# Kernel optimization log

Hardware: AMD Instinct MI355X
Metric: run time of the kernel (lower is better)

The kernel has to match this reference:

```python
import jax, jax.numpy as jnp
import numpy as np

D_MODEL = 1024
NUM_HEADS = 16
ROPE_THETA = 10000.0


def setup_inputs() -> dict:
    key = jax.random.key(0)
    ks = jax.random.split(key, 5)
    B, S, D = 4, 2048, D_MODEL
    std = (2.0 / (D * D)) ** 0.5
    return {
        "x": jax.random.normal(ks[0], (B, S, D), dtype=jnp.float32),
        "Wq": jax.random.normal(ks[1], (D, D), dtype=jnp.float32) * std,
        "Wk": jax.random.normal(ks[2], (D, D), dtype=jnp.float32) * std,
        "Wv": jax.random.normal(ks[3], (D, D), dtype=jnp.float32) * std,
        "Wo": jax.random.normal(ks[4], (D, D), dtype=jnp.float32) * std,
    }


def _apply_rope(t, sin, cos):
    # t: [B, H, S, d_k]; sin/cos: [S, d_k//2] (broadcast over B, H)
    e = t[..., 0::2]
    o = t[..., 1::2]
    rot = jnp.stack((e * cos - o * sin, e * sin + o * cos), axis=-1)
    return rot.reshape(t.shape)  # interleave back to d_k


def reference(x, Wq, Wk, Wv, Wo):
    B, S, D = x.shape
    H = NUM_HEADS
    dk = D // H

    def proj(W):
        y = jnp.einsum('bsd,ed->bse', x, W)  # Linear: weight is [out, in]
        return y.reshape(B, S, H, dk).transpose(0, 2, 1, 3)  # [B,H,S,dk]

    q, k, v = proj(Wq), proj(Wk), proj(Wv)

    # RoPE cache (token_positions = arange(S))
    half = dk // 2
    inv_freq = 1.0 / (ROPE_THETA ** (jnp.arange(half, dtype=jnp.float32) * 2.0 / dk))
    angles = jnp.arange(S, dtype=jnp.float32)[:, None] * inv_freq[None, :]  # [S, half]
    sin, cos = jnp.sin(angles), jnp.cos(angles)
    q = _apply_rope(q, sin, cos)
    k = _apply_rope(k, sin, cos)

    # scaled dot-product attention with causal mask
    scores = jnp.einsum('bhqd,bhkd->bhqk', q, k) / jnp.sqrt(jnp.float32(dk))
    causal = jnp.tril(jnp.ones((S, S), dtype=bool))
    scores = jnp.where(causal, scores, jnp.finfo(scores.dtype).min)
    p = jax.nn.softmax(scores, axis=-1)
    out = jnp.einsum('bhqk,bhkd->bhqd', p, v)  # [B,H,S,dk]

    out = out.transpose(0, 2, 1, 3).reshape(B, S, D)
    return jnp.einsum('bsd,ed->bse', out, Wo)
```

## Files before the change

### kernel.cpp

```cpp
#include <hip/hip_runtime.h>

typedef unsigned short u16;
typedef unsigned int   u32;

typedef short    short8 __attribute__((ext_vector_type(8)));
typedef __bf16   bf16x8 __attribute__((ext_vector_type(8)));
typedef _Float16 half8  __attribute__((ext_vector_type(8)));
typedef float    f32x4  __attribute__((ext_vector_type(4)));

#define S_LEN   2048
#define DM      1024
#define NHEAD   16
#define DK      64
#define KDIM    1024

__device__ __forceinline__ u16 f2bf(float f) {
    u32 u = __builtin_bit_cast(u32, f);
    u += 0x7FFFu + ((u >> 16) & 1u);
    return (u16)(u >> 16);
}
__device__ __forceinline__ f32x4 mfma_bf16(short8 a, short8 b, f32x4 c) {
    return __builtin_amdgcn_mfma_f32_16x16x32_bf16(
        __builtin_bit_cast(bf16x8, a), __builtin_bit_cast(bf16x8, b), c, 0, 0, 0);
}
__device__ __forceinline__ f32x4 mfma_f16(half8 a, half8 b, f32x4 c) {
    return __builtin_amdgcn_mfma_f32_16x16x32_f16(a, b, c, 0, 0, 0);
}
__device__ __forceinline__ u32 pk_f16(float a, float b) {
    return __builtin_bit_cast(u32, __builtin_amdgcn_cvt_pkrtz(a, b));
}
__device__ __forceinline__ void gl_lds16(const void* g, void* l) {
    __builtin_amdgcn_global_load_lds(
        (const __attribute__((address_space(1))) u32*)g,
        (__attribute__((address_space(3))) u32*)l, 16, 0, 0);
}
__device__ __forceinline__ void bar_raw() { asm volatile("s_barrier" ::: "memory"); }
__device__ __forceinline__ void wait_vm4() { asm volatile("s_waitcnt vmcnt(4)" ::: "memory"); }
__device__ __forceinline__ void wait_vm0() { asm volatile("s_waitcnt vmcnt(0)" ::: "memory"); }

__device__ __forceinline__ int perm_inv(int rc) {
    const int nt = rc >> 4, mid = (rc >> 2) & 3, r = rc & 3;
    return 32 * (nt >> 1) + 8 * mid + 4 * (nt & 1) + r;
}

__global__ void cvt_all(const float4* __restrict__ x,  const float4* __restrict__ Wq,
                        const float4* __restrict__ Wk, const float4* __restrict__ Wv,
                        const float4* __restrict__ Wo,
                        uint2* __restrict__ oX, uint2* __restrict__ oWcat,
                        uint2* __restrict__ oWo,
                        float* __restrict__ sT, float* __restrict__ cT) {
    const int i = blockIdx.x * 256 + threadIdx.x;
    if (i < 3145728) {
        const float4* in;
        uint2* out;
        if (i < 2097152) {
            in = x + i;  out = oX + i;
        } else {
            const int j = i - 2097152;
            const int w = j >> 18, k = j & 262143;
            in  = (w == 0 ? Wq : w == 1 ? Wk : w == 2 ? Wv : Wo) + k;
            out = (w < 3) ? (oWcat + w * 262144 + k) : (oWo + k);
        }
        float4 f = *in;
        uint2 o;
        o.x = (u32)f2bf(f.x) | ((u32)f2bf(f.y) << 16);
        o.y = (u32)f2bf(f.z) | ((u32)f2bf(f.w) << 16);
        *out = o;
    } else {
        const int idx = i - 3145728;
        const float fi = expf(-(float)(idx >> 11) * 0.287823136624255f);
        const float ang = (float)(idx & 2047) * fi;
        sT[idx] = sinf(ang);
        cT[idx] = cosf(ang);
    }
}

template <int MODE>
__global__ __launch_bounds__(256)
void gemm_nt(const u16* __restrict__ A, const u16* __restrict__ Bw,
             u16* __restrict__ oQ, u16* __restrict__ oK, u16* __restrict__ oVt,
             float* __restrict__ oF,
             const float* __restrict__ ropeS, const float* __restrict__ ropeC) {
    __shared__ u16 As[2][128 * 32];
    __shared__ u16 Bs[2][128 * 32];
    const int tid  = threadIdx.x;
    const int wave = tid >> 6, lane = tid & 63;
    const int quad = lane >> 4, l15 = lane & 15;
    const int wr = wave >> 1, wc = wave & 1;
    const int NX  = (MODE == 0) ? 24 : 8;
    const int lin = (int)blockIdx.x + NX * (int)blockIdx.y;
    const int xcd = lin & 7, idx = lin >> 3;
    const int mbase = (xcd * 8 + idx / NX) * 128;
    const int nbase = (idx % NX) * 128;

    f32x4 acc[4][4];
#pragma unroll
    for (int i = 0; i < 4; i++)
#pragma unroll
        for (int j = 0; j < 4; j++) acc[i][j] = (f32x4)0.0f;

    const int srow0 = wave * 32 + (lane >> 2);
    const int srow1 = srow0 + 16;
    const int scolb = ((lane & 3) ^ ((lane >> 3) & 3)) * 16;
    const int ldsOff = wave * 2048 + lane * 16;
    const u16* gA0 = A  + (size_t)(mbase + srow0) * KDIM;
    const u16* gA1 = A  + (size_t)(mbase + srow1) * KDIM;
    const u16* gB0 = Bw + (size_t)(nbase + srow0) * KDIM;
    const u16* gB1 = Bw + (size_t)(nbase + srow1) * KDIM;
    const int koffq = (quad ^ ((l15 >> 1) & 3)) * 8;

    gl_lds16((const char*)gA0 + scolb, (char*)As[0] + ldsOff);
    gl_lds16((const char*)gA1 + scolb, (char*)As[0] + ldsOff + 1024);
    gl_lds16((const char*)gB0 + scolb, (char*)Bs[0] + ldsOff);
    gl_lds16((const char*)gB1 + scolb, (char*)Bs[0] + ldsOff + 1024);

    const int KT = KDIM / 32;
    for (int kt = 0; kt < KT; kt++) {
        const int cur = kt & 1, nxt = cur ^ 1;
        const int kkn = ((kt + 1 < KT) ? (kt + 1) : kt) * 32;
        bar_raw();
        gl_lds16((const char*)(gA0 + kkn) + scolb, (char*)As[nxt] + ldsOff);
        gl_lds16((const char*)(gA1 + kkn) + scolb, (char*)As[nxt] + ldsOff + 1024);
        gl_lds16((const char*)(gB0 + kkn) + scolb, (char*)Bs[nxt] + ldsOff);
        gl_lds16((const char*)(gB1 + kkn) + scolb, (char*)Bs[nxt] + ldsOff + 1024);
        wait_vm4();
        bar_raw();

        short8 af[4], bf[4];
#pragma unroll
        for (int mt = 0; mt < 4; mt++)
            af[mt] = *(const short8*)&As[cur][(wr * 64 + mt * 16 + l15) * 32 + koffq];
#pragma unroll
        for (int nt = 0; nt < 4; nt++)
            bf[nt] = *(const short8*)&Bs[cur][(wc * 64 + nt * 16 + l15) * 32 + koffq];
#pragma unroll
        for (int mt = 0; mt < 4; mt++)
#pragma unroll
            for (int nt = 0; nt < 4; nt++)
                acc[mt][nt] = mfma_bf16(af[mt], bf[nt], acc[mt][nt]);
    }
    wait_vm0();

    const int proj_blk = (MODE == 0) ? (nbase >> 10) : 2;

    const float* sB[4];
    const float* cB[4];
    if (MODE == 0 && proj_blk < 2) {
#pragma unroll
        for (int nt = 0; nt < 4; nt++) {
            const int fi = nt * 8 + (l15 >> 1);
            sB[nt] = ropeS + fi * 2048;
            cB[nt] = ropeC + fi * 2048;
        }
    }
    const int par = l15 & 1;

#pragma unroll
    for (int mt = 0; mt < 4; mt++) {
#pragma unroll
        for (int nt = 0; nt < 4; nt++) {
            const int n  = nbase + wc * 64 + nt * 16 + l15;
            const int mb = mbase + wr * 64 + mt * 16 + quad * 4;
            f32x4 v = acc[mt][nt];
            if (MODE == 0) {
                const int e = n & 1023;
                const int h = e >> 6, d = e & 63;
                if (proj_blk == 2) {
                    const int b_ = mb >> 11, s = mb & 2047;
                    const int bh = b_ * NHEAD + h;
                    uint2 pk;
                    pk.x = pk_f16(v[0], v[1]);
                    pk.y = pk_f16(v[2], v[3]);
                    *(uint2*)&oVt[((size_t)bh * DK + d) * S_LEN + s] = pk;
                } else {
                    u16* dst = (proj_blk == 0) ? oQ : oK;
                    float vp[4];
#pragma unroll
                    for (int r = 0; r < 4; r++) vp[r] = __shfl_xor(v[r], 1);
                    const int b_ = mb >> 11, s0 = mb & 2047;
                    const int bh = b_ * NHEAD + h;
                    const f32x4 sn = *(const f32x4*)(sB[nt] + s0);
                    const f32x4 cs = *(const f32x4*)(cB[nt] + s0);
#pragma unroll
                    for (int r = 0; r < 4; r++) {
                        const float res = par ? (vp[r] * sn[r] + v[r] * cs[r])
                                              : (v[r] * cs[r] - vp[r] * sn[r]);
                        dst[((size_t)bh * S_LEN + (s0 + r)) * DK + d] = f2bf(res);
                    }
                }
            } else {
#pragma unroll
                for (int r = 0; r < 4; r++)
                    oF[(size_t)(mb + r) * DM + n] = v[r];
            }
        }
    }
}

__global__ __launch_bounds__(256)
void flash_attn(const u16* __restrict__ Q, const u16* __restrict__ K,
                const u16* __restrict__ Vt, u16* __restrict__ Oc) {
    __shared__ u16 Ks[2][64 * 64];
    __shared__ u16 Vs[2][64 * 64];
    const int lin = (int)blockIdx.x + 64 * (int)blockIdx.y;
    const int xcd = lin & 7, idx = lin >> 3;
    const int bh  = xcd * 8 + (idx & 7);
    const int qt  = 15 - (idx >> 3);
    const int tid  = threadIdx.x;
    const int wave = tid >> 6, lane = tid & 63;
    const int quad = lane >> 4, l15 = lane & 15;
    const int x7 = l15 & 7;
    const size_t headQK = (size_t)bh * S_LEN * DK;
    const size_t headVt = (size_t)bh * DK * S_LEN;
    const int b = bh >> 4, h = bh & 15;
    const float SCL = 0.18033688011112042f;

    half8 ones;
#pragma unroll
    for (int j = 0; j < 8; j++) ones[j] = (_Float16)1.0f;

    const int rwl  = lane >> 3;
    const int scol = (lane & 7) ^ rwl;
    const int rc0 = wave * 16 + rwl, rc1 = rc0 + 8;
    const u16* gK0 = K  + headQK + (size_t)perm_inv(rc0) * DK + scol * 8;
    const u16* gK1 = K  + headQK + (size_t)perm_inv(rc1) * DK + scol * 8;
    const u16* gV0 = Vt + headVt + (size_t)rc0 * S_LEN + scol * 8;
    const u16* gV1 = Vt + headVt + (size_t)rc1 * S_LEN + scol * 8;
    const int ldsOff = wave * 2048 + lane * 16;
    const int koff0 = (quad ^ x7) * 8;
    const int koff1 = ((4 + quad) ^ x7) * 8;

    short8 qf[2][2];
#pragma unroll
    for (int hh = 0; hh < 2; hh++) {
        const int qrow = qt * 128 + hh * 64 + wave * 16 + l15;
        qf[hh][0] = *(const short8*)&Q[headQK + (size_t)qrow * DK + quad * 8];
        qf[hh][1] = *(const short8*)&Q[headQK + (size_t)qrow * DK + 32 + quad * 8];
    }

    float m_st[2];
    f32x4 lacc[2];
    f32x4 oacc[2][4];
#pragma unroll
    for (int hh = 0; hh < 2; hh++) {
        m_st[hh] = -__builtin_inff();
        lacc[hh] = (f32x4)0.0f;
#pragma unroll
        for (int n = 0; n < 4; n++) oacc[hh][n] = (f32x4)0.0f;
    }

    const int NT = 2 * qt + 2;
    gl_lds16(gK0, (char*)Ks[0] + ldsOff);
    gl_lds16(gK1, (char*)Ks[0] + ldsOff + 1024);
    gl_lds16(gV0, (char*)Vs[0] + ldsOff);
    gl_lds16(gV1, (char*)Vs[0] + ldsOff + 1024);

    for (int kt = 0; kt < NT; kt++) {
        const int cur = kt & 1, nxt = cur ^ 1;
        bar_raw();
        {
            const int ktn = (kt + 1 < NT) ? kt + 1 : kt;
            gl_lds16(gK0 + (size_t)ktn * 64 * DK, (char*)Ks[nxt] + ldsOff);
            gl_lds16(gK1 + (size_t)ktn * 64 * DK, (char*)Ks[nxt] + ldsOff + 1024);
            gl_lds16(gV0 + ktn * 64,              (char*)Vs[nxt] + ldsOff);
            gl_lds16(gV1 + ktn * 64,              (char*)Vs[nxt] + ldsOff + 1024);
        }
        wait_vm4();
        bar_raw();

        const bool act0 = (kt != 2 * qt + 1);

        f32x4 sc[2][4];
        __builtin_amdgcn_s_setprio(1);
#pragma unroll
        for (int nt = 0; nt < 4; nt++) {
            const int rb = (nt * 16 + l15) * 64;
            short8 kf0 = *(const short8*)&Ks[cur][rb + koff0];
            short8 kf1 = *(const short8*)&Ks[cur][rb + koff1];
            f32x4 z0 = (f32x4)0.0f, z1 = (f32x4)0.0f;
            z0 = mfma_bf16(kf0, qf[0][0], z0);
            z0 = mfma_bf16(kf1, qf[0][1], z0);
            z1 = mfma_bf16(kf0, qf[1][0], z1);
            z1 = mfma_bf16(kf1, qf[1][1], z1);
#pragma unroll
            for (int r = 0; r < 4; r++) { z0[r] *= SCL; z1[r] *= SCL; }
            sc[0][nt] = z0;
            sc[1][nt] = z1;
        }
        __builtin_amdgcn_s_setprio(0);

        half8 pf[2][2];
        float alr[2][4];
#pragma unroll
        for (int hh = 0; hh < 2; hh++) {
            if (hh == 0 && !act0) continue;
            if (kt == 2 * qt + hh) {
                const int qloc = wave * 16 + l15;
#pragma unroll
                for (int nt = 0; nt < 4; nt++) {
                    const int kb = 32 * (nt >> 1) + 8 * quad + 4 * (nt & 1);
#pragma unroll
                    for (int r = 0; r < 4; r++)
                        if (kb + r > qloc) sc[hh][nt][r] = -__builtin_inff();
                }
            }
            float mx0 = fmaxf(fmaxf(sc[hh][0][0], sc[hh][0][1]), fmaxf(sc[hh][0][2], sc[hh][0][3]));
            float mx1 = fmaxf(fmaxf(sc[hh][1][0], sc[hh][1][1]), fmaxf(sc[hh][1][2], sc[hh][1][3]));
            float mx2 = fmaxf(fmaxf(sc[hh][2][0], sc[hh][2][1]), fmaxf(sc[hh][2][2], sc[hh][2][3]));
            float mx3 = fmaxf(fmaxf(sc[hh][3][0], sc[hh][3][1]), fmaxf(sc[hh][3][2], sc[hh][3][3]));
            float mx = fmaxf(fmaxf(mx0, mx1), fmaxf(mx2, mx3));
            mx = fmaxf(mx, __shfl_xor(mx, 16));
            mx = fmaxf(mx, __shfl_xor(mx, 32));
            const float mn = fmaxf(m_st[hh], mx);
            const float alpha = __builtin_amdgcn_exp2f(m_st[hh] - mn);
            m_st[hh] = mn;
#pragma unroll
            for (int nt = 0; nt < 4; nt++)
#pragma unroll
                for (int r = 0; r < 4; r++)
                    sc[hh][nt][r] = __builtin_amdgcn_exp2f(sc[hh][nt][r] - m_st[hh]);
            u32 pw[8];
            pw[0] = pk_f16(sc[hh][0][0], sc[hh][0][1]); pw[1] = pk_f16(sc[hh][0][2], sc[hh][0][3]);
            pw[2] = pk_f16(sc[hh][1][0], sc[hh][1][1]); pw[3] = pk_f16(sc[hh][1][2], sc[hh][1][3]);
            pw[4] = pk_f16(sc[hh][2][0], sc[hh][2][1]); pw[5] = pk_f16(sc[hh][2][2], sc[hh][2][3]);
            pw[6] = pk_f16(sc[hh][3][0], sc[hh][3][1]); pw[7] = pk_f16(sc[hh][3][2], sc[hh][3][3]);
            pf[hh][0] = __builtin_bit_cast(half8, *(uint4*)&pw[0]);
            pf[hh][1] = __builtin_bit_cast(half8, *(uint4*)&pw[4]);
#pragma unroll
            for (int r = 0; r < 4; r++) alr[hh][r] = __shfl(alpha, quad * 20 + r);
#pragma unroll
            for (int n = 0; n < 4; n++)
#pragma unroll
                for (int r = 0; r < 4; r++) oacc[hh][n][r] *= alr[hh][r];
#pragma unroll
            for (int r = 0; r < 4; r++) lacc[hh][r] *= alr[hh][r];
        }

        __builtin_amdgcn_s_setprio(1);
#pragma unroll
        for (int c = 0; c < 2; c++) {
            if (act0) lacc[0] = mfma_f16(pf[0][c], ones, lacc[0]);
            lacc[1] = mfma_f16(pf[1][c], ones, lacc[1]);
            const int voff = ((c * 4 + quad) ^ x7) * 8;
#pragma unroll
            for (int nt2 = 0; nt2 < 4; nt2++) {
                half8 vf = __builtin_bit_cast(half8,
                    *(const short8*)&Vs[cur][(nt2 * 16 + l15) * 64 + voff]);
                if (act0) oacc[0][nt2] = mfma_f16(pf[0][c], vf, oacc[0][nt2]);
                oacc[1][nt2] = mfma_f16(pf[1][c], vf, oacc[1][nt2]);
            }
        }
        __builtin_amdgcn_s_setprio(0);
    }
    wait_vm0();

#pragma unroll
    for (int hh = 0; hh < 2; hh++) {
#pragma unroll
        for (int r = 0; r < 4; r++) {
            const float inv = 1.0f / lacc[hh][r];
            const int s = qt * 128 + hh * 64 + wave * 16 + quad * 4 + r;
#pragma unroll
            for (int nt2 = 0; nt2 < 4; nt2++)
                Oc[((size_t)(b * S_LEN + s)) * DM + h * 64 + nt2 * 16 + l15] =
                    f2bf(oacc[hh][nt2][r] * inv);
        }
    }
}

#define OFF_XBF   ((size_t)0)
#define OFF_WCAT  ((size_t)8388608)
#define OFF_WO    ((size_t)11534336)
#define OFF_QB    ((size_t)12582912)
#define OFF_KB    ((size_t)20971520)
#define OFF_VT    ((size_t)29360128)
#define OFF_ROPE  ((size_t)37748736)

extern "C" void kernel_launch(void* const* d_in, const int* in_sizes, int n_in,
                              void* d_out, int out_size, void* d_ws, size_t ws_size,
                              hipStream_t stream) {
    const float* x  = (const float*)d_in[0];
    const float* Wq = (const float*)d_in[1];
    const float* Wk = (const float*)d_in[2];
    const float* Wv = (const float*)d_in[3];
    const float* Wo = (const float*)d_in[4];
    u16* ws  = (u16*)d_ws;
    u16* XBF = ws + OFF_XBF;
    u16* WCA = ws + OFF_WCAT;
    u16* WOB = ws + OFF_WO;
    u16* QB  = ws + OFF_QB;
    u16* KB  = ws + OFF_KB;
    u16* VT  = ws + OFF_VT;
    float* ropeS = (float*)(ws + OFF_ROPE);
    float* ropeC = ropeS + 65536;
    u16* AT  = XBF;

    cvt_all<<<12544, 256, 0, stream>>>((const float4*)x, (const float4*)Wq,
                                       (const float4*)Wk, (const float4*)Wv,
                                       (const float4*)Wo,
                                       (uint2*)XBF, (uint2*)WCA, (uint2*)WOB,
                                       ropeS, ropeC);

    gemm_nt<0><<<dim3(24, 64), 256, 0, stream>>>(XBF, WCA, QB, KB, VT, nullptr,
                                                 ropeS, ropeC);
    flash_attn<<<dim3(64, 16), 256, 0, stream>>>(QB, KB, VT, AT);
    gemm_nt<1><<<dim3(8, 64), 256, 0, stream>>>(AT, WOB, nullptr, nullptr, nullptr,
                                                (float*)d_out, nullptr, nullptr);
}
```

Before: 269.9 us.

## Replace double-buffered prefetch with single-stage 64-wide K tiles

```diff
diff --git a/kernel.cpp b/kernel.cpp
--- a/kernel.cpp
+++ b/kernel.cpp
@@ -109,37 +109,38 @@
     const u16* gB1 = Bw + (size_t)(nbase + srow1) * KDIM;
     const int koffq = (quad ^ ((l15 >> 1) & 3)) * 8;
 
-    gl_lds16((const char*)gA0 + scolb, (char*)As[0] + ldsOff);
-    gl_lds16((const char*)gA1 + scolb, (char*)As[0] + ldsOff + 1024);
-    gl_lds16((const char*)gB0 + scolb, (char*)Bs[0] + ldsOff);
-    gl_lds16((const char*)gB1 + scolb, (char*)Bs[0] + ldsOff + 1024);
-
-    const int KT = KDIM / 32;
+    const int KT = KDIM / 64;
     for (int kt = 0; kt < KT; kt++) {
-        const int cur = kt & 1, nxt = cur ^ 1;
-        const int kkn = ((kt + 1 < KT) ? (kt + 1) : kt) * 32;
-        bar_raw();
-        gl_lds16((const char*)(gA0 + kkn) + scolb, (char*)As[nxt] + ldsOff);
-        gl_lds16((const char*)(gA1 + kkn) + scolb, (char*)As[nxt] + ldsOff + 1024);
-        gl_lds16((const char*)(gB0 + kkn) + scolb, (char*)Bs[nxt] + ldsOff);
-        gl_lds16((const char*)(gB1 + kkn) + scolb, (char*)Bs[nxt] + ldsOff + 1024);
-        wait_vm4();
-        bar_raw();
-
-        short8 af[4], bf[4];
-#pragma unroll
-        for (int mt = 0; mt < 4; mt++)
-            af[mt] = *(const short8*)&As[cur][(wr * 64 + mt * 16 + l15) * 32 + koffq];
-#pragma unroll
-        for (int nt = 0; nt < 4; nt++)
-            bf[nt] = *(const short8*)&Bs[cur][(wc * 64 + nt * 16 + l15) * 32 + koffq];
-#pragma unroll
-        for (int mt = 0; mt < 4; mt++)
+        const int kk = kt * 64;
+        __syncthreads();
+#pragma unroll
+        for (int s = 0; s < 2; s++) {
+            const int ko = kk + s * 32;
+            gl_lds16((const char*)(gA0 + ko) + scolb, (char*)As[s] + ldsOff);
+            gl_lds16((const char*)(gA1 + ko) + scolb, (char*)As[s] + ldsOff + 1024);
+            gl_lds16((const char*)(gB0 + ko) + scolb, (char*)Bs[s] + ldsOff);
+            gl_lds16((const char*)(gB1 + ko) + scolb, (char*)Bs[s] + ldsOff + 1024);
+        }
+        __syncthreads();
+
+        short8 af[4][2], bf[4][2];
+#pragma unroll
+        for (int s = 0; s < 2; s++) {
+#pragma unroll
+            for (int mt = 0; mt < 4; mt++)
+                af[mt][s] = *(const short8*)&As[s][(wr * 64 + mt * 16 + l15) * 32 + koffq];
 #pragma unroll
             for (int nt = 0; nt < 4; nt++)
-                acc[mt][nt] = mfma_bf16(af[mt], bf[nt], acc[mt][nt]);
-    }
-    wait_vm0();
+                bf[nt][s] = *(const short8*)&Bs[s][(wc * 64 + nt * 16 + l15) * 32 + koffq];
+        }
+#pragma unroll
+        for (int s = 0; s < 2; s++)
+#pragma unroll
+            for (int mt = 0; mt < 4; mt++)
+#pragma unroll
+                for (int nt = 0; nt < 4; nt++)
+                    acc[mt][nt] = mfma_bf16(af[mt][s], bf[nt][s], acc[mt][nt]);
+    }
 
     const int proj_blk = (MODE == 0) ? (nbase >> 10) : 2;
 
```

Measured after the change: 266.8 us. No clear change (-1.1%).
